# Performance work log

Hardware: AMD Instinct MI355X
Metric: run time of the kernel (lower is better)

Reference implementation:

```python
import jax, jax.numpy as jnp
import numpy as np

S = 3072        # total tokens (3 images x 1024 patches)
E = 1280        # n_embed
H = 16          # n_heads
HD = E // H     # head_dim = 80
NSEG = 3


def rotate_half(x):
    x1 = x[..., : x.shape[-1] // 2]
    x2 = x[..., x.shape[-1] // 2 :]
    return jnp.concatenate((-x2, x1), axis=-1)


def setup_inputs() -> dict:
    key = jax.random.key(0)
    ks = jax.random.split(key, 6)
    x = jax.random.normal(ks[0], (S, E), dtype=jnp.float32)
    rotary_pos_emb = jax.random.normal(ks[1], (S, HD // 2), dtype=jnp.float32)
    qkv_w = jax.random.normal(ks[2], (3 * E, E), dtype=jnp.float32) * 0.02
    qkv_b = jax.random.normal(ks[3], (3 * E,), dtype=jnp.float32) * 0.02
    proj_w = jax.random.normal(ks[4], (E, E), dtype=jnp.float32) * 0.02
    proj_b = jax.random.normal(ks[5], (E,), dtype=jnp.float32) * 0.02
    cu_seqlens = (jnp.arange(NSEG + 1, dtype=jnp.int32) * (S // NSEG))  # [0,1024,2048,3072]
    return {"x": x, "rotary_pos_emb": rotary_pos_emb, "qkv_w": qkv_w,
            "qkv_b": qkv_b, "proj_w": proj_w, "proj_b": proj_b,
            "cu_seqlens": cu_seqlens}


def reference(x, rotary_pos_emb, qkv_w, qkv_b, proj_w, proj_b, cu_seqlens):
    seq_len = x.shape[0]
    # qkv projection (torch Linear: x @ W.T + b)
    qkv = (x @ qkv_w.T + qkv_b).reshape(seq_len, 3, H, HD)
    q, k, v = qkv[:, 0], qkv[:, 1], qkv[:, 2]          # each [S, H, HD]

    # inline RoPE: cos/sin repeated over the two halves of head_dim
    cos = jnp.cos(rotary_pos_emb)
    sin = jnp.sin(rotary_pos_emb)
    cos = jnp.concatenate([cos, cos], axis=-1)[:, None, :]  # [S, 1, HD]
    sin = jnp.concatenate([sin, sin], axis=-1)[:, None, :]
    q = q * cos + rotate_half(q) * sin
    k = k * cos + rotate_half(k) * sin

    # block-diagonal segment mask from cu_seqlens
    seg = jnp.searchsorted(cu_seqlens, jnp.arange(seq_len), side="right")  # [S]
    mask = seg[:, None] == seg[None, :]                 # [S, S] bool

    scale = jnp.asarray(1.0 / np.sqrt(HD), dtype=q.dtype)
    scores = jnp.einsum("qhd,khd->hqk", q, k) * scale   # [H, S, S]
    scores = jnp.where(mask[None], scores, jnp.finfo(scores.dtype).min)
    attn = jax.nn.softmax(scores, axis=-1)
    out = jnp.einsum("hqk,khd->qhd", attn, v).reshape(seq_len, E)
    return out @ proj_w.T + proj_b
```

## Files before the change

kernel.cpp:

```cpp
#include <hip/hip_runtime.h>
#include <hip/hip_bf16.h>
#include <math.h>

#define SEQ   3072
#define EMB   1280
#define NHEAD 16
#define HDIM  80
#define QKVN  3840
#define NSEGS 3

typedef __attribute__((ext_vector_type(8))) short bf16x8;
typedef __attribute__((ext_vector_type(4))) short bf16x4;
typedef __attribute__((ext_vector_type(4))) float f32x4;

__device__ __forceinline__ short f2bf(float f) {
    __hip_bfloat16 h = __float2bfloat16(f);
    return *reinterpret_cast<short*>(&h);
}
__device__ __forceinline__ float bf2f(short s) {
    unsigned int u = ((unsigned int)(unsigned short)s) << 16;
    union { unsigned int u; float f; } c; c.u = u;
    return c.f;
}

__device__ __forceinline__ void gload_lds16(const void* g, void* l) {
    __builtin_amdgcn_global_load_lds(
        (const __attribute__((address_space(1))) unsigned int*)g,
        (__attribute__((address_space(3))) unsigned int*)l, 16, 0, 0);
}

__global__ __launch_bounds__(256)
void cvt3_kernel(const float* __restrict__ a, short* __restrict__ oa, int na8,
                 const float* __restrict__ b, short* __restrict__ ob, int nb8,
                 const float* __restrict__ c, short* __restrict__ oc, int nc8)
{
    int j = blockIdx.x * 256 + threadIdx.x;
    const float* src; short* dst;
    if (j < na8) { src = a; dst = oa; }
    else if ((j -= na8) < nb8) { src = b; dst = ob; }
    else { j -= nb8; src = c; dst = oc; }
    float4 x = *reinterpret_cast<const float4*>(&src[j*8]);
    float4 y = *reinterpret_cast<const float4*>(&src[j*8+4]);
    bf16x8 o;
    o[0]=f2bf(x.x); o[1]=f2bf(x.y); o[2]=f2bf(x.z); o[3]=f2bf(x.w);
    o[4]=f2bf(y.x); o[5]=f2bf(y.y); o[6]=f2bf(y.z); o[7]=f2bf(y.w);
    *reinterpret_cast<bf16x8*>(&dst[j*8]) = o;
}

__device__ __forceinline__ void store_val(float v, float* p) { *p = v; }
__device__ __forceinline__ void store_val(float v, short* p) { *p = f2bf(v); }

template<typename OT>
__global__ __launch_bounds__(256)
void gemm_bf16_nt(const short* __restrict__ A, int lda,
                  const short* __restrict__ B,
                  const float* __restrict__ bias, OT* __restrict__ C,
                  int M, int N, int K)
{
    __shared__ short As[128][32];
    __shared__ short Bs[128][32];

    const int tid = threadIdx.x;
    const int w   = tid >> 6;
    const int l   = tid & 63;
    const int l15 = l & 15;
    const int l4  = l >> 4;
    const int wr  = w >> 1;
    const int wc  = w & 1;
    const int row0 = blockIdx.y * 128;
    const int col0 = blockIdx.x * 128;

    const int srow = l >> 2;
    const int sk   = (l & 3) * 8;

    f32x4 acc[4][4];
    #pragma unroll
    for (int mi = 0; mi < 4; ++mi)
        #pragma unroll
        for (int ni = 0; ni < 4; ++ni) acc[mi][ni] = (f32x4){0.f,0.f,0.f,0.f};

    for (int k0 = 0; k0 < K; k0 += 32) {
        {
            const int c0 = w, c1 = w + 4;
            gload_lds16(&A[(size_t)(row0 + c0*16 + srow) * lda + k0 + sk], &As[c0*16][0]);
            gload_lds16(&A[(size_t)(row0 + c1*16 + srow) * lda + k0 + sk], &As[c1*16][0]);
            gload_lds16(&B[(size_t)(col0 + c0*16 + srow) * K   + k0 + sk], &Bs[c0*16][0]);
            gload_lds16(&B[(size_t)(col0 + c1*16 + srow) * K   + k0 + sk], &Bs[c1*16][0]);
        }
        __syncthreads();

        bf16x8 af[4], bfr[4];
        #pragma unroll
        for (int mi = 0; mi < 4; ++mi)
            af[mi] = *reinterpret_cast<const bf16x8*>(&As[wr*64 + mi*16 + l15][l4*8]);
        #pragma unroll
        for (int ni = 0; ni < 4; ++ni)
            bfr[ni] = *reinterpret_cast<const bf16x8*>(&Bs[wc*64 + ni*16 + l15][l4*8]);

        #pragma unroll
        for (int mi = 0; mi < 4; ++mi)
            #pragma unroll
            for (int ni = 0; ni < 4; ++ni)
                acc[mi][ni] = __builtin_amdgcn_mfma_f32_16x16x32_bf16(
                    af[mi], bfr[ni], acc[mi][ni], 0, 0, 0);
        __syncthreads();
    }

    #pragma unroll
    for (int ni = 0; ni < 4; ++ni) {
        int col = col0 + wc*64 + ni*16 + l15;
        float bv = bias[col];
        #pragma unroll
        for (int mi = 0; mi < 4; ++mi) {
            #pragma unroll
            for (int r = 0; r < 4; ++r) {
                size_t row = (size_t)(row0 + wr*64 + mi*16 + l4*4 + r);
                store_val(acc[mi][ni][r] + bv, &C[row * (size_t)N + col]);
            }
        }
    }
}

template<typename OT>
__global__ __launch_bounds__(256)
void gemm_bf16_nt64(const short* __restrict__ A, int lda,
                    const short* __restrict__ B,
                    const float* __restrict__ bias, OT* __restrict__ C,
                    int M, int N, int K)
{
    __shared__ short As[128][32];
    __shared__ short Bs[64][32];

    const int tid = threadIdx.x;
    const int w   = tid >> 6;
    const int l   = tid & 63;
    const int l15 = l & 15;
    const int l4  = l >> 4;
    const int wr  = w >> 1;
    const int wc  = w & 1;
    const int row0 = blockIdx.y * 128;
    const int col0 = blockIdx.x * 64;

    const int srow = l >> 2;
    const int sk   = (l & 3) * 8;

    f32x4 acc[4][2];
    #pragma unroll
    for (int mi = 0; mi < 4; ++mi)
        #pragma unroll
        for (int ni = 0; ni < 2; ++ni) acc[mi][ni] = (f32x4){0.f,0.f,0.f,0.f};

    for (int k0 = 0; k0 < K; k0 += 32) {
        {
            const int c0 = w, c1 = w + 4;
            gload_lds16(&A[(size_t)(row0 + c0*16 + srow) * lda + k0 + sk], &As[c0*16][0]);
            gload_lds16(&A[(size_t)(row0 + c1*16 + srow) * lda + k0 + sk], &As[c1*16][0]);
            gload_lds16(&B[(size_t)(col0 + w*16  + srow) * K   + k0 + sk], &Bs[w*16][0]);
        }
        __syncthreads();

        bf16x8 af[4], bfr[2];
        #pragma unroll
        for (int mi = 0; mi < 4; ++mi)
            af[mi] = *reinterpret_cast<const bf16x8*>(&As[wr*64 + mi*16 + l15][l4*8]);
        #pragma unroll
        for (int ni = 0; ni < 2; ++ni)
            bfr[ni] = *reinterpret_cast<const bf16x8*>(&Bs[wc*32 + ni*16 + l15][l4*8]);

        #pragma unroll
        for (int mi = 0; mi < 4; ++mi)
            #pragma unroll
            for (int ni = 0; ni < 2; ++ni)
                acc[mi][ni] = __builtin_amdgcn_mfma_f32_16x16x32_bf16(
                    af[mi], bfr[ni], acc[mi][ni], 0, 0, 0);
        __syncthreads();
    }

    #pragma unroll
    for (int ni = 0; ni < 2; ++ni) {
        int col = col0 + wc*32 + ni*16 + l15;
        float bv = bias[col];
        #pragma unroll
        for (int mi = 0; mi < 4; ++mi) {
            #pragma unroll
            for (int r = 0; r < 4; ++r) {
                size_t row = (size_t)(row0 + wr*64 + mi*16 + l4*4 + r);
                store_val(acc[mi][ni][r] + bv, &C[row * (size_t)N + col]);
            }
        }
    }
}

__global__ __launch_bounds__(256)
void rope_bf16_kernel(short* __restrict__ qkv, const float* __restrict__ rpe)
{
    int idx = blockIdx.x * 256 + threadIdx.x;
    int blk = idx % 5;
    int h   = (idx / 5) % NHEAD;
    int s   = (idx / (5*NHEAD)) % SEQ;
    int t   = idx / (5*NHEAD*SEQ);
    int d0  = blk * 8;

    const float* rp = rpe + s*40 + d0;
    short* p = qkv + (size_t)s*QKVN + t*EMB + h*HDIM + d0;
    bf16x8 v0 = *reinterpret_cast<const bf16x8*>(p);
    bf16x8 v1 = *reinterpret_cast<const bf16x8*>(p + 40);
    bf16x8 o0, o1;
    #pragma unroll
    for (int j = 0; j < 8; ++j) {
        float ang = rp[j];
        float sn = sinf(ang), cs = cosf(ang);
        float a = bf2f(v0[j]), b = bf2f(v1[j]);
        o0[j] = f2bf(a*cs - b*sn);
        o1[j] = f2bf(b*cs + a*sn);
    }
    *reinterpret_cast<bf16x8*>(p)      = o0;
    *reinterpret_cast<bf16x8*>(p + 40) = o1;
}

__global__ __launch_bounds__(256)
void attn_mfma(const short* __restrict__ qkv, const int* __restrict__ cu,
               short* __restrict__ aout)
{
    const int flat = blockIdx.x;
    const int xcd  = flat & 7;
    const int rem  = flat >> 3;
    const int qt   = rem & 15;
    const int shhi = rem >> 4;
    const int sh   = xcd + 8*shhi;
    const int h    = sh / 3;
    const int seg  = sh - 3*h;
    const int s0 = cu[seg], s1 = cu[seg+1];

    const int tid = threadIdx.x;
    const int w   = tid >> 6;
    const int l   = tid & 63;
    const int l15 = l & 15;
    const int l4  = l >> 4;

    __shared__ short Kl[64][128];
    __shared__ short Vt[HDIM][64];

    const int q0 = s0 + qt*64 + w*16;

    bf16x8 bzero;
    #pragma unroll
    for (int j = 0; j < 8; ++j) bzero[j] = 0;

    bf16x8 qf[3];
    {
        const short* qp = qkv + (size_t)(q0 + l15) * QKVN + h*HDIM;
        qf[0] = *reinterpret_cast<const bf16x8*>(qp + l4*8);
        qf[1] = *reinterpret_cast<const bf16x8*>(qp + 32 + l4*8);
        qf[2] = (l4 < 2) ? *reinterpret_cast<const bf16x8*>(qp + 64 + l4*8) : bzero;
    }

    float m = -3.4e38f, lsum = 0.f;
    f32x4 O[5];
    #pragma unroll
    for (int dt = 0; dt < 5; ++dt) O[dt] = (f32x4){0.f,0.f,0.f,0.f};

    int kkey[3], ku[3];
    const short* kptr[3];
    short* klds[3];
    #pragma unroll
    for (int i = 0; i < 3; ++i) {
        int task = tid + i*256;
        kkey[i] = task / 12;
        ku[i]   = task - kkey[i]*12;
        kptr[i] = qkv + (size_t)(s0 + kkey[i])*QKVN + EMB + h*HDIM + ku[i]*8;
        klds[i] = &Kl[kkey[i]][(ku[i] ^ (kkey[i] & 7))*8];
    }

    const int u1  = ((l >> 2) & 3) | ((l >> 5) << 2);
    const int bs1 = ((l >> 4) & 1) * 4 + (l & 3);
    const int k2  = w*16 + l15;
    const int u2  = ((k2 >> 2) & 3) | ((k2 >> 5) << 2);
    const int bs2 = ((k2 >> 4) & 1) * 4 + (k2 & 3);
    const bool sec = (l < 16);

    const short* vp1 = qkv + (size_t)(s0 + l)  * QKVN + 2*EMB + h*HDIM + w*16;
    const short* vp2 = qkv + (size_t)(s0 + k2) * QKVN + 2*EMB + h*HDIM + 64;

    bf16x8 kreg[3];
    bf16x8 vregA, vregB, vregC, vregD;
    #pragma unroll
    for (int i = 0; i < 3; ++i)
        kreg[i] = (ku[i] < 10) ? *reinterpret_cast<const bf16x8*>(kptr[i]) : bzero;
    vregA = *reinterpret_cast<const bf16x8*>(vp1);
    vregB = *reinterpret_cast<const bf16x8*>(vp1 + 8);
    if (sec) {
        vregC = *reinterpret_cast<const bf16x8*>(vp2);
        vregD = *reinterpret_cast<const bf16x8*>(vp2 + 8);
    }

    const float scale2 = 0.1612982054f;
    const int nk = s1 - s0;
    const size_t step = (size_t)64 * QKVN;
    short* vt_flat = &Vt[0][0];

    for (int kc = 0; kc < nk; kc += 64) {
        __syncthreads();

        #pragma unroll
        for (int i = 0; i < 3; ++i)
            *reinterpret_cast<bf16x8*>(klds[i]) = kreg[i];
        {
            const int rb = w*16*64;
            #pragma unroll
            for (int i = 0; i < 8; ++i) {
                vt_flat[rb + i*64      + ((u1 ^ i)       & 7)*8 + bs1] = vregA[i];
                vt_flat[rb + (i+8)*64  + ((u1 ^ i)       & 7)*8 + bs1] = vregB[i];
            }
            if (sec) {
                #pragma unroll
                for (int i = 0; i < 8; ++i) {
                    vt_flat[(64+i)*64  + ((u2 ^ i)       & 7)*8 + bs2] = vregC[i];
                    vt_flat[(72+i)*64  + ((u2 ^ i)       & 7)*8 + bs2] = vregD[i];
                }
            }
        }

        if (kc + 64 < nk) {
            #pragma unroll
            for (int i = 0; i < 3; ++i) {
                kptr[i] += step;
                if (ku[i] < 10) kreg[i] = *reinterpret_cast<const bf16x8*>(kptr[i]);
            }
            vp1 += step; vp2 += step;
            vregA = *reinterpret_cast<const bf16x8*>(vp1);
            vregB = *reinterpret_cast<const bf16x8*>(vp1 + 8);
            if (sec) {
                vregC = *reinterpret_cast<const bf16x8*>(vp2);
                vregD = *reinterpret_cast<const bf16x8*>(vp2 + 8);
            }
        }
        __syncthreads();

        f32x4 S[4];
        __builtin_amdgcn_s_setprio(1);
        #pragma unroll
        for (int ct = 0; ct < 4; ++ct) {
            f32x4 acc = (f32x4){0.f,0.f,0.f,0.f};
            int key = ct*16 + l15;
            #pragma unroll
            for (int t = 0; t < 3; ++t) {
                int u = (4*t + l4) ^ (key & 7);
                bf16x8 a = *reinterpret_cast<const bf16x8*>(&Kl[key][u*8]);
                acc = __builtin_amdgcn_mfma_f32_16x16x32_bf16(a, qf[t], acc, 0, 0, 0);
            }
            S[ct] = acc;
        }
        __builtin_amdgcn_s_setprio(0);

        float mxr = -3.4e38f;
        #pragma unroll
        for (int ct = 0; ct < 4; ++ct)
            #pragma unroll
            for (int r = 0; r < 4; ++r) mxr = fmaxf(mxr, S[ct][r]);
        float mx = mxr * scale2;
        mx = fmaxf(mx, __shfl_xor(mx, 16));
        mx = fmaxf(mx, __shfl_xor(mx, 32));
        if (!__all(mx - m <= 8.f)) {
            float mn   = fmaxf(m, mx);
            float corr = exp2f(m - mn);
            lsum *= corr;
            #pragma unroll
            for (int dt = 0; dt < 5; ++dt)
                #pragma unroll
                for (int r = 0; r < 4; ++r) O[dt][r] *= corr;
            m = mn;
        }
        float p[4][4];
        float ps = 0.f;
        #pragma unroll
        for (int ct = 0; ct < 4; ++ct)
            #pragma unroll
            for (int r = 0; r < 4; ++r) {
                float e = exp2f(fmaf(S[ct][r], scale2, -m));
                p[ct][r] = e;
                ps += e;
            }
        ps += __shfl_xor(ps, 16);
        ps += __shfl_xor(ps, 32);
        lsum += ps;

        #pragma unroll
        for (int s2 = 0; s2 < 2; ++s2) {
            bf16x8 pb;
            #pragma unroll
            for (int j = 0; j < 8; ++j)
                pb[j] = f2bf(p[2*s2 + (j>>2)][j & 3]);
            __builtin_amdgcn_s_setprio(1);
            #pragma unroll
            for (int dt = 0; dt < 5; ++dt) {
                int d = dt*16 + l15;
                bf16x8 va = *reinterpret_cast<const bf16x8*>(
                    &vt_flat[d*64 + (((4*s2 + l4) ^ (d & 7)) & 7)*8]);
                O[dt] = __builtin_amdgcn_mfma_f32_16x16x32_bf16(va, pb, O[dt], 0, 0, 0);
            }
            __builtin_amdgcn_s_setprio(0);
        }
    }

    float inv = 1.f / lsum;
    short* orow = aout + (size_t)(q0 + l15) * EMB + h*HDIM;
    #pragma unroll
    for (int dt = 0; dt < 5; ++dt) {
        bf16x4 o4;
        #pragma unroll
        for (int r = 0; r < 4; ++r) o4[r] = f2bf(O[dt][r] * inv);
        *reinterpret_cast<bf16x4*>(&orow[dt*16 + 4*l4]) = o4;
    }
}

extern "C" void kernel_launch(void* const* d_in, const int* in_sizes, int n_in,
                              void* d_out, int out_size, void* d_ws, size_t ws_size,
                              hipStream_t stream)
{
    const float* x      = (const float*)d_in[0];
    const float* rpe    = (const float*)d_in[1];
    const float* qkv_w  = (const float*)d_in[2];
    const float* qkv_b  = (const float*)d_in[3];
    const float* proj_w = (const float*)d_in[4];
    const float* proj_b = (const float*)d_in[5];
    const int*   cu     = (const int*)d_in[6];
    float* out = (float*)d_out;

    short* ws       = (short*)d_ws;
    short* qkv_bf   = ws;
    short* x_bf     = qkv_bf  + (size_t)SEQ * QKVN;
    short* qkvw_bf  = x_bf    + (size_t)SEQ * EMB;
    short* projw_bf = qkvw_bf + (size_t)QKVN * EMB;
    short* attn_bf  = projw_bf+ (size_t)EMB * EMB;

    dim3 blk(256);

    const int na8 = SEQ*EMB/8, nb8 = QKVN*EMB/8, nc8 = EMB*EMB/8;
    cvt3_kernel<<<dim3((na8+nb8+nc8)/256), blk, 0, stream>>>(
        x, x_bf, na8, qkv_w, qkvw_bf, nb8, proj_w, projw_bf, nc8);

    gemm_bf16_nt<short><<<dim3(QKVN/128, SEQ/128), blk, 0, stream>>>(
        x_bf, EMB, qkvw_bf, qkv_b, qkv_bf, SEQ, QKVN, EMB);

    rope_bf16_kernel<<<dim3(2*SEQ*NHEAD*5/256), blk, 0, stream>>>(qkv_bf, rpe);

    attn_mfma<<<dim3(16*NSEGS*NHEAD), blk, 0, stream>>>(qkv_bf, cu, attn_bf);

    gemm_bf16_nt64<float><<<dim3(EMB/64, SEQ/128), blk, 0, stream>>>(
        attn_bf, EMB, projw_bf, proj_b, out, SEQ, EMB, EMB);
}
```

Baseline: 144.7 us.

## Split attention key range in two and merge partials in a combine kernel

Each attention block now handles only half of its segment's keys, which doubles the grid from 768 to 1536 blocks. Each block writes an unnormalized bf16 partial output plus its running max and sum. A new combine kernel rescales the two partials with exp2 weights, normalizes them and writes the final attention output. The aim is more parallelism and better latency hiding in the attention stage. The cost is an extra launch, extra global traffic for the partials, and one more bf16 rounding of the unnormalized output. The workspace regions for x and the qkv weights are reused to hold the partials.

Result: slower. 150.4 us (+4.0%).

```diff
diff --git a/kernel.cpp b/kernel.cpp
--- a/kernel.cpp
+++ b/kernel.cpp
@@ -220,17 +220,24 @@
 
 __global__ __launch_bounds__(256)
 void attn_mfma(const short* __restrict__ qkv, const int* __restrict__ cu,
-               short* __restrict__ aout)
-{
-    const int flat = blockIdx.x;
-    const int xcd  = flat & 7;
-    const int rem  = flat >> 3;
-    const int qt   = rem & 15;
-    const int shhi = rem >> 4;
-    const int sh   = xcd + 8*shhi;
-    const int h    = sh / 3;
-    const int seg  = sh - 3*h;
+               short* __restrict__ part0, short* __restrict__ part1,
+               float* __restrict__ ml)
+{
+    const int flat  = blockIdx.x;
+    const int xcd   = flat & 7;
+    const int rem   = flat >> 3;
+    const int qt    = rem & 15;
+    const int rem2  = rem >> 4;
+    const int split = rem2 & 1;
+    const int shhi  = rem2 >> 1;
+    const int sh    = xcd + 8*shhi;
+    const int h     = sh / 3;
+    const int seg   = sh - 3*h;
     const int s0 = cu[seg], s1 = cu[seg+1];
+
+    const int half = (((s1 - s0) >> 1) + 63) & ~63;
+    const int sbeg = s0 + split*half;
+    const int send = split ? s1 : (s0 + half);
 
     const int tid = threadIdx.x;
     const int w   = tid >> 6;
@@ -268,7 +275,7 @@
         int task = tid + i*256;
         kkey[i] = task / 12;
         ku[i]   = task - kkey[i]*12;
-        kptr[i] = qkv + (size_t)(s0 + kkey[i])*QKVN + EMB + h*HDIM + ku[i]*8;
+        kptr[i] = qkv + (size_t)(sbeg + kkey[i])*QKVN + EMB + h*HDIM + ku[i]*8;
         klds[i] = &Kl[kkey[i]][(ku[i] ^ (kkey[i] & 7))*8];
     }
 
@@ -279,8 +286,8 @@
     const int bs2 = ((k2 >> 4) & 1) * 4 + (k2 & 3);
     const bool sec = (l < 16);
 
-    const short* vp1 = qkv + (size_t)(s0 + l)  * QKVN + 2*EMB + h*HDIM + w*16;
-    const short* vp2 = qkv + (size_t)(s0 + k2) * QKVN + 2*EMB + h*HDIM + 64;
+    const short* vp1 = qkv + (size_t)(sbeg + l)  * QKVN + 2*EMB + h*HDIM + w*16;
+    const short* vp2 = qkv + (size_t)(sbeg + k2) * QKVN + 2*EMB + h*HDIM + 64;
 
     bf16x8 kreg[3];
     bf16x8 vregA, vregB, vregC, vregD;
@@ -295,11 +302,11 @@
     }
 
     const float scale2 = 0.1612982054f;
-    const int nk = s1 - s0;
+    const int nkl = send - sbeg;
     const size_t step = (size_t)64 * QKVN;
     short* vt_flat = &Vt[0][0];
 
-    for (int kc = 0; kc < nk; kc += 64) {
+    for (int kc = 0; kc < nkl; kc += 64) {
         __syncthreads();
 
         #pragma unroll
@@ -321,7 +328,7 @@
             }
         }
 
-        if (kc + 64 < nk) {
+        if (kc + 64 < nkl) {
             #pragma unroll
             for (int i = 0; i < 3; ++i) {
                 kptr[i] += step;
@@ -403,15 +410,45 @@
         }
     }
 
-    float inv = 1.f / lsum;
-    short* orow = aout + (size_t)(q0 + l15) * EMB + h*HDIM;
+    short* part = split ? part1 : part0;
+    short* orow = part + (size_t)(q0 + l15) * EMB + h*HDIM;
     #pragma unroll
     for (int dt = 0; dt < 5; ++dt) {
         bf16x4 o4;
         #pragma unroll
-        for (int r = 0; r < 4; ++r) o4[r] = f2bf(O[dt][r] * inv);
+        for (int r = 0; r < 4; ++r) o4[r] = f2bf(O[dt][r]);
         *reinterpret_cast<bf16x4*>(&orow[dt*16 + 4*l4]) = o4;
     }
+    if (l4 == 0) {
+        float* mlrow = ml + ((size_t)(q0 + l15) * NHEAD + h) * 4 + split*2;
+        mlrow[0] = m;
+        mlrow[1] = lsum;
+    }
+}
+
+__global__ __launch_bounds__(256)
+void combine_kernel(const short* __restrict__ p0, const short* __restrict__ p1,
+                    const float* __restrict__ ml, short* __restrict__ outp)
+{
+    int j = blockIdx.x * 256 + threadIdx.x;
+    int row  = j / 160;
+    int grp  = j - row*160;
+    int head = grp / 10;
+
+    const float* mlp = ml + ((size_t)row * NHEAD + head) * 4;
+    float m0 = mlp[0], l0 = mlp[1], m1 = mlp[2], l1 = mlp[3];
+    float M  = fmaxf(m0, m1);
+    float w0 = exp2f(m0 - M), w1 = exp2f(m1 - M);
+    float inv = 1.f / (w0*l0 + w1*l1);
+    w0 *= inv; w1 *= inv;
+
+    bf16x8 a = *reinterpret_cast<const bf16x8*>(&p0[(size_t)j*8]);
+    bf16x8 b = *reinterpret_cast<const bf16x8*>(&p1[(size_t)j*8]);
+    bf16x8 o;
+    #pragma unroll
+    for (int i = 0; i < 8; ++i)
+        o[i] = f2bf(w0*bf2f(a[i]) + w1*bf2f(b[i]));
+    *reinterpret_cast<bf16x8*>(&outp[(size_t)j*8]) = o;
 }
 
 extern "C" void kernel_launch(void* const* d_in, const int* in_sizes, int n_in,
@@ -433,6 +470,9 @@
     short* qkvw_bf  = x_bf    + (size_t)SEQ * EMB;
     short* projw_bf = qkvw_bf + (size_t)QKVN * EMB;
     short* attn_bf  = projw_bf+ (size_t)EMB * EMB;
+    short* part0    = x_bf;
+    short* part1    = qkvw_bf;
+    float* ml       = (float*)(qkvw_bf + (size_t)SEQ*EMB);
 
     dim3 blk(256);
 
@@ -445,7 +485,11 @@
 
     rope_bf16_kernel<<<dim3(2*SEQ*NHEAD*5/256), blk, 0, stream>>>(qkv_bf, rpe);
 
-    attn_mfma<<<dim3(16*NSEGS*NHEAD), blk, 0, stream>>>(qkv_bf, cu, attn_bf);
+    attn_mfma<<<dim3(16*2*NSEGS*NHEAD), blk, 0, stream>>>(
+        qkv_bf, cu, part0, part1, ml);
+
+    combine_kernel<<<dim3(SEQ*EMB/8/256), blk, 0, stream>>>(
+        part0, part1, ml, attn_bf);
 
     gemm_bf16_nt64<float><<<dim3(EMB/64, SEQ/128), blk, 0, stream>>>(
         attn_bf, EMB, projw_bf, proj_b, out, SEQ, EMB, EMB);
```
